# Performance work log

Hardware: AMD Instinct MI355X
Metric: run time of the kernel (lower is better)

The kernel has to match this reference:

```python
import jax, jax.numpy as jnp
import numpy as np

H = 8        # heads
DH = 64      # dim_head
EPS = 1e-5   # LayerNorm eps (torch default)


def setup_inputs() -> dict:
    key = jax.random.key(0)
    k0, k1, k2, k3, k4 = jax.random.split(key, 5)
    b, l, n, dim = 2, 8, 256, 512
    inner = H * DH
    return {
        "xyzs": jax.random.normal(k0, (b, l, n, 3), dtype=jnp.float32),
        "features": jax.random.normal(k1, (b, l, n, dim), dtype=jnp.float32),
        "ln_gamma": jnp.ones((dim,), dtype=jnp.float32),
        "ln_beta": jnp.zeros((dim,), dtype=jnp.float32),
        "w_qkv": jax.random.normal(k2, (dim, 3 * inner), dtype=jnp.float32) * 0.02,
        "w_sp": jax.random.normal(k3, (3, DH), dtype=jnp.float32) * 0.3,
        "w_out": jax.random.normal(k4, (inner, dim), dtype=jnp.float32) * 0.02,
        "b_out": jnp.zeros((dim,), dtype=jnp.float32),
    }


def reference(xyzs, features, ln_gamma, ln_beta, w_qkv, w_sp, w_out, b_out):
    b, l, n, dim = features.shape
    m = l * n
    inner = H * DH
    scale = DH ** (-0.5)

    # LayerNorm over last dim (biased variance, eps=1e-5)
    mu = jnp.mean(features, axis=-1, keepdims=True)
    var = jnp.var(features, axis=-1, keepdims=True)
    normed = (features - mu) * jax.lax.rsqrt(var + EPS) * ln_gamma + ln_beta

    # qkv projection, chunk into q,k,v, reshape 'b l n (h d) -> b h (l n) d'
    qkv = normed.reshape(b, m, dim) @ w_qkv            # [b, m, 3*inner]
    def split_heads(t):
        return t.reshape(b, m, H, DH).transpose(0, 2, 1, 3)  # [b, h, m, d]
    q = split_heads(qkv[..., :inner])
    k = split_heads(qkv[..., inner:2 * inner])
    v = split_heads(qkv[..., 2 * inner:])

    dots = jnp.einsum('bhid,bhjd->bhij', q, k) * scale  # [b, h, m, m]
    attn = jax.nn.softmax(dots, axis=-1)
    v_out = jnp.einsum('bhij,bhjd->bhid', attn, v)      # [b, h, m, d]

    # pairwise coordinate deltas: delta[b,i,j,c] = xyz[b,j,c] - xyz[b,i,c]
    xyz_f = xyzs.reshape(b, m, 3)
    delta = xyz_f[:, None, :, :] - xyz_f[:, :, None, :]  # [b, m, m, 3]
    # attention-weighted aggregation over j (avoids [b,h,m,m,3] intermediate)
    agg = jnp.einsum('bhij,bijc->bhic', attn, delta)     # [b, h, m, 3]
    disp = agg @ w_sp                                    # [b, h, m, DH]

    out = v_out + disp                                   # [b, h, m, DH]
    out = out.transpose(0, 2, 1, 3).reshape(b, m, inner) # 'b h m d -> b m (h d)'
    out = jax.nn.gelu(out @ w_out + b_out, approximate=False)
    return out.reshape(b, l, n, dim) + features
```

## Files before the change

kernel.cpp:

```cpp
#include <hip/hip_runtime.h>
#include <hip/hip_bf16.h>
#include <math.h>

#define BB   2
#define MM   2048
#define DIM  512
#define NH   8
#define DHd  64
#define NQK  1536
#define ROWS 4096
#define NROW 32768

typedef __hip_bfloat16 bf16;
typedef __attribute__((ext_vector_type(8))) short bf16x8;
typedef __attribute__((ext_vector_type(4))) float f32x4;
typedef __attribute__((ext_vector_type(8))) unsigned short us8;

__device__ __forceinline__ unsigned short f2bf_bits(float x) {
    bf16 h = __float2bfloat16(x);
    return *(unsigned short*)&h;
}
__device__ __forceinline__ float bf2f(unsigned short u) {
    unsigned int v = ((unsigned int)u) << 16;
    return __uint_as_float(v);
}

__global__ __launch_bounds__(256) void transpose_bf16_fused(
    const float* __restrict__ wqkv, const float* __restrict__ wout,
    unsigned short* __restrict__ wqkvT, unsigned short* __restrict__ woutT)
{
    __shared__ float st[64][65];
    int by = blockIdx.y;
    const float* in; unsigned short* out; int N, n0;
    if (by < 24) { in = wqkv; out = wqkvT; N = NQK; n0 = by * 64; }
    else         { in = wout; out = woutT; N = DIM; n0 = (by - 24) * 64; }
    int k0 = blockIdx.x * 64;
    int tid = threadIdx.x;
    #pragma unroll
    for (int p = 0; p < 16; p++) {
        int e = tid + p * 256;
        int r = e >> 6, c = e & 63;
        st[r][c] = in[(size_t)(k0 + r) * N + n0 + c];
    }
    __syncthreads();
    #pragma unroll
    for (int p = 0; p < 16; p++) {
        int e = tid + p * 256;
        int nr = e >> 6, kc = e & 63;
        out[(size_t)(n0 + nr) * DIM + k0 + kc] = f2bf_bits(st[kc][nr]);
    }
}

__global__ __launch_bounds__(256) void ln_kernel(
    const float* __restrict__ feat, const float* __restrict__ gamma,
    const float* __restrict__ beta, unsigned short* __restrict__ normed)
{
    int row = blockIdx.x;
    int tid = threadIdx.x;
    const float* fr = feat + (size_t)row * DIM;
    float x0 = fr[tid];
    float x1 = fr[tid + 256];
    float s  = x0 + x1;
    float ss = x0 * x0 + x1 * x1;
    #pragma unroll
    for (int o = 32; o >= 1; o >>= 1) { s += __shfl_down(s, o); ss += __shfl_down(ss, o); }
    __shared__ float ws_[4], wss_[4];
    int wid = tid >> 6, lane = tid & 63;
    if (lane == 0) { ws_[wid] = s; wss_[wid] = ss; }
    __syncthreads();
    if (tid == 0) {
        float a = 0.f, b = 0.f;
        for (int i = 0; i < 4; i++) { a += ws_[i]; b += wss_[i]; }
        ws_[0] = a; wss_[0] = b;
    }
    __syncthreads();
    float mu  = ws_[0] * (1.0f / DIM);
    float var = wss_[0] * (1.0f / DIM) - mu * mu;
    float inv = rsqrtf(var + 1e-5f);
    normed[(size_t)row * DIM + tid]       = f2bf_bits((x0 - mu) * inv * gamma[tid] + beta[tid]);
    normed[(size_t)row * DIM + tid + 256] = f2bf_bits((x1 - mu) * inv * gamma[tid + 256] + beta[tid + 256]);
}

__global__ __launch_bounds__(256) void qkv_gemm(
    const unsigned short* __restrict__ A, const unsigned short* __restrict__ BT,
    unsigned short* __restrict__ qd, unsigned short* __restrict__ kd,
    unsigned short* __restrict__ vd)
{
    __shared__ __align__(16) unsigned short sA[128 * 40];
    __shared__ __align__(16) unsigned short sB[128 * 40];
    int tid = threadIdx.x;
    int r0 = blockIdx.x * 128;
    int n0 = blockIdx.y * 128;
    int chunk = n0 >> 9;
    int cl    = n0 & 511;
    int w = tid >> 6, lane = tid & 63;
    int wm = w >> 1, wn = w & 1;
    int ln15 = lane & 15, quad = lane >> 4;

    int srow = tid >> 1;
    int scol = (tid & 1) * 16;

    f32x4 acc[4][4] = {};

    for (int k0 = 0; k0 < DIM; k0 += 32) {
        __syncthreads();
        *(us8*)&sA[srow * 40 + scol]     = *(const us8*)&A[(size_t)(r0 + srow) * DIM + k0 + scol];
        *(us8*)&sA[srow * 40 + scol + 8] = *(const us8*)&A[(size_t)(r0 + srow) * DIM + k0 + scol + 8];
        *(us8*)&sB[srow * 40 + scol]     = *(const us8*)&BT[(size_t)(n0 + srow) * DIM + k0 + scol];
        *(us8*)&sB[srow * 40 + scol + 8] = *(const us8*)&BT[(size_t)(n0 + srow) * DIM + k0 + scol + 8];
        __syncthreads();
        const unsigned short* fa = (chunk == 2) ? sA : sB;
        const unsigned short* fb = (chunk == 2) ? sB : sA;
        bf16x8 af[4], bf_[4];
        #pragma unroll
        for (int i = 0; i < 4; i++)
            af[i] = *(const bf16x8*)&fa[(wm * 64 + i * 16 + ln15) * 40 + quad * 8];
        #pragma unroll
        for (int j = 0; j < 4; j++)
            bf_[j] = *(const bf16x8*)&fb[(wn * 64 + j * 16 + ln15) * 40 + quad * 8];
        #pragma unroll
        for (int i = 0; i < 4; i++)
            #pragma unroll
            for (int j = 0; j < 4; j++)
                acc[i][j] = __builtin_amdgcn_mfma_f32_16x16x32_bf16(af[i], bf_[j], acc[i][j], 0, 0, 0);
    }

    if (chunk == 2) {
        int rowb = r0 + wm * 64 + quad * 4;
        #pragma unroll
        for (int j = 0; j < 4; j++) {
            int c = cl + wn * 64 + j * 16 + ln15;
            int h = c >> 6, d = c & 63;
            #pragma unroll
            for (int i = 0; i < 4; i++) {
                int gr = rowb + i * 16;
                int bb = gr >> 11, mm = gr & 2047;
                ushort4 pk;
                pk.x = f2bf_bits(acc[i][j][0]);
                pk.y = f2bf_bits(acc[i][j][1]);
                pk.z = f2bf_bits(acc[i][j][2]);
                pk.w = f2bf_bits(acc[i][j][3]);
                *(ushort4*)&vd[((size_t)(bb * NH + h) * DHd + d) * MM + mm] = pk;
            }
        }
    } else {
        unsigned short* dst = (chunk == 0) ? qd : kd;
        float sc = (chunk == 0) ? 0.125f : 1.0f;
        #pragma unroll
        for (int i = 0; i < 4; i++) {
            int within0 = cl + wm * 64 + i * 16 + quad * 4;
            int h = within0 >> 6, d = within0 & 63;
            #pragma unroll
            for (int j = 0; j < 4; j++) {
                int gr = r0 + wn * 64 + j * 16 + ln15;
                int bb = gr >> 11, mm = gr & 2047;
                ushort4 pk;
                pk.x = f2bf_bits(acc[i][j][0] * sc);
                pk.y = f2bf_bits(acc[i][j][1] * sc);
                pk.z = f2bf_bits(acc[i][j][2] * sc);
                pk.w = f2bf_bits(acc[i][j][3] * sc);
                *(ushort4*)&dst[((size_t)(bb * NH + h) * MM + mm) * DHd + d] = pk;
            }
        }
    }
}

__global__ __launch_bounds__(256) void attn_kernel(
    const unsigned short* __restrict__ qg, const unsigned short* __restrict__ kg,
    const unsigned short* __restrict__ vg, const float* __restrict__ xyzs,
    unsigned short* __restrict__ obuf, float* __restrict__ lbuf)
{
    __shared__ __align__(16) unsigned short sQ[64 * 72];
    __shared__ __align__(16) unsigned short sK[64 * 72];
    __shared__ __align__(16) unsigned short sVT[80 * 72];
    __shared__ __align__(16) unsigned short sP[64 * 72];

    int tid = threadIdx.x;
    int bh = blockIdx.y; int bb = bh >> 3;
    int i0 = blockIdx.x * 64;
    int ks = blockIdx.z;
    int w = tid >> 6;
    int lane = tid & 63;
    int ln15 = lane & 15;
    int quad = lane >> 4;

    for (int e = tid; e < 12 * 72; e += 256) sVT[68 * 72 + e] = 0;
    if (tid < 64) sVT[67 * 72 + tid] = 0x3F80;

    {
        const unsigned short* src = qg + ((size_t)bh * MM + i0) * DHd;
        int row = tid >> 2, col = (tid & 3) * 16;
        *(us8*)&sQ[row * 72 + col]     = *(const us8*)&src[(size_t)tid * 16];
        *(us8*)&sQ[row * 72 + col + 8] = *(const us8*)&src[(size_t)tid * 16 + 8];
    }
    asm volatile("s_waitcnt lgkmcnt(0)" ::: "memory");
    bf16x8 aq0 = *(const bf16x8*)&sQ[(w * 16 + ln15) * 72 + quad * 8];
    bf16x8 aq1 = *(const bf16x8*)&sQ[(w * 16 + ln15) * 72 + 32 + quad * 8];

    f32x4 o[5] = {};

    const unsigned short* kbase = kg + (size_t)bh * MM * DHd;
    const unsigned short* vbase = vg + (size_t)bh * DHd * MM;
    int jbeg = ks * (MM / 2), jend = jbeg + (MM / 2);

    int swzr = (ln15 >> 2) << 4;
    int pr0 = (quad * 8) ^ swzr;
    int pr1 = (32 + quad * 8) ^ swzr;
    int pwb = quad << 4;

    for (int jt = jbeg; jt < jend; jt += 64) {
        __syncthreads();
        {
            const unsigned short* src = kbase + (size_t)jt * DHd;
            int row = tid >> 2, col = (tid & 3) * 16;
            *(us8*)&sK[row * 72 + col]     = *(const us8*)&src[(size_t)tid * 16];
            *(us8*)&sK[row * 72 + col + 8] = *(const us8*)&src[(size_t)tid * 16 + 8];
        }
        {
            const unsigned short* src = vbase + jt;
            int d = tid >> 2, koff = (tid & 3) * 16;
            *(us8*)&sVT[d * 72 + koff]     = *(const us8*)&src[(size_t)d * MM + koff];
            *(us8*)&sVT[d * 72 + koff + 8] = *(const us8*)&src[(size_t)d * MM + koff + 8];
        }
        if (tid < 192) {
            int key = tid / 3, c = tid - key * 3;
            float x = xyzs[((size_t)bb * MM + jt) * 3 + tid];
            sVT[(64 + c) * 72 + key] = f2bf_bits(x);
        }
        __syncthreads();

        f32x4 sacc[4];
        #pragma unroll
        for (int t = 0; t < 4; t++) {
            bf16x8 bk0 = *(const bf16x8*)&sK[(t * 16 + ln15) * 72 + quad * 8];
            bf16x8 bk1 = *(const bf16x8*)&sK[(t * 16 + ln15) * 72 + 32 + quad * 8];
            f32x4 z = {};
            z = __builtin_amdgcn_mfma_f32_16x16x32_bf16(aq0, bk0, z, 0, 0, 0);
            z = __builtin_amdgcn_mfma_f32_16x16x32_bf16(aq1, bk1, z, 0, 0, 0);
            sacc[t] = z;
        }

        #pragma unroll
        for (int t = 0; t < 4; t++) {
            int colb = (t * 16) ^ pwb;
            #pragma unroll
            for (int reg = 0; reg < 4; reg++) {
                float pv = __expf(sacc[t][reg]);
                sP[(w * 16 + quad * 4 + reg) * 72 + colb + ln15] = f2bf_bits(pv);
            }
        }
        asm volatile("s_waitcnt lgkmcnt(0)" ::: "memory");
        bf16x8 ap0 = *(const bf16x8*)&sP[(w * 16 + ln15) * 72 + pr0];
        bf16x8 ap1 = *(const bf16x8*)&sP[(w * 16 + ln15) * 72 + pr1];
        #pragma unroll
        for (int t = 0; t < 5; t++) {
            bf16x8 bv0 = *(const bf16x8*)&sVT[(t * 16 + ln15) * 72 + quad * 8];
            bf16x8 bv1 = *(const bf16x8*)&sVT[(t * 16 + ln15) * 72 + 32 + quad * 8];
            o[t] = __builtin_amdgcn_mfma_f32_16x16x32_bf16(ap0, bv0, o[t], 0, 0, 0);
            o[t] = __builtin_amdgcn_mfma_f32_16x16x32_bf16(ap1, bv1, o[t], 0, 0, 0);
        }
    }

    size_t kso = (size_t)ks * NROW;
    #pragma unroll
    for (int reg = 0; reg < 4; reg++) {
        size_t row = (size_t)bh * MM + i0 + w * 16 + quad * 4 + reg;
        unsigned short* orow = obuf + (kso + row) * 72;
        #pragma unroll
        for (int t = 0; t < 4; t++)
            orow[t * 16 + ln15] = f2bf_bits(o[t][reg]);
        if (ln15 < 3)  orow[64 + ln15] = f2bf_bits(o[4][reg]);
        if (ln15 == 3) lbuf[kso + row] = o[4][reg];
    }
}

__global__ __launch_bounds__(256) void merge_kernel(
    const unsigned short* __restrict__ obuf, const float* __restrict__ lbuf,
    const float* __restrict__ xyzs, const float* __restrict__ wsp,
    unsigned short* __restrict__ attn_out)
{
    __shared__ float sW[3][64];
    int tid = threadIdx.x;
    if (tid < 192) sW[tid >> 6][tid & 63] = wsp[tid];
    __syncthreads();
    int r   = blockIdx.x * 64 + (tid >> 2);
    int d0  = (tid & 3) * 16;
    int bh = r >> 11, qrow = r & 2047, bb = bh >> 3, hh = bh & 7;
    const unsigned short* p1 = obuf + (size_t)r * 72;
    const unsigned short* p2 = obuf + ((size_t)NROW + r) * 72;
    float invl = 1.f / (lbuf[r] + lbuf[NROW + r]);
    size_t xb = ((size_t)bb * MM + qrow) * 3;
    float gx = (bf2f(p1[64]) + bf2f(p2[64])) * invl - xyzs[xb + 0];
    float gy = (bf2f(p1[65]) + bf2f(p2[65])) * invl - xyzs[xb + 1];
    float gz = (bf2f(p1[66]) + bf2f(p2[66])) * invl - xyzs[xb + 2];
    us8 a0 = *(const us8*)&p1[d0];
    us8 a1 = *(const us8*)&p1[d0 + 8];
    us8 b0 = *(const us8*)&p2[d0];
    us8 b1 = *(const us8*)&p2[d0 + 8];
    unsigned short outv[16];
    #pragma unroll
    for (int e = 0; e < 8; e++) {
        int d = d0 + e;
        float v = (bf2f(a0[e]) + bf2f(b0[e])) * invl
                + gx * sW[0][d] + gy * sW[1][d] + gz * sW[2][d];
        outv[e] = f2bf_bits(v);
    }
    #pragma unroll
    for (int e = 0; e < 8; e++) {
        int d = d0 + 8 + e;
        float v = (bf2f(a1[e]) + bf2f(b1[e])) * invl
                + gx * sW[0][d] + gy * sW[1][d] + gz * sW[2][d];
        outv[8 + e] = f2bf_bits(v);
    }
    unsigned short* dst = attn_out + ((size_t)bb * MM + qrow) * DIM + hh * DHd + d0;
    *(us8*)dst       = *(us8*)&outv[0];
    *(us8*)(dst + 8) = *(us8*)&outv[8];
}

__global__ __launch_bounds__(256) void out_gemm(
    const unsigned short* __restrict__ A, const unsigned short* __restrict__ BT,
    const float* __restrict__ bias, const float* __restrict__ feat,
    float* __restrict__ out)
{
    __shared__ __align__(16) unsigned short sA[128 * 40];
    __shared__ __align__(16) unsigned short sB[64 * 40];
    int tid = threadIdx.x;
    int r0 = blockIdx.x * 128, n0 = blockIdx.y * 64;
    int w = tid >> 6, lane = tid & 63;
    int ln15 = lane & 15, quad = lane >> 4;

    int srowA = tid >> 1, scolA = (tid & 1) * 16;
    int srowB = tid >> 2, scolB = (tid & 3) * 8;

    f32x4 acc[2][4] = {};

    for (int k0 = 0; k0 < DIM; k0 += 32) {
        __syncthreads();
        *(us8*)&sA[srowA * 40 + scolA]     = *(const us8*)&A[(size_t)(r0 + srowA) * DIM + k0 + scolA];
        *(us8*)&sA[srowA * 40 + scolA + 8] = *(const us8*)&A[(size_t)(r0 + srowA) * DIM + k0 + scolA + 8];
        *(us8*)&sB[srowB * 40 + scolB]     = *(const us8*)&BT[(size_t)(n0 + srowB) * DIM + k0 + scolB];
        __syncthreads();
        bf16x8 af[2], bf_[4];
        #pragma unroll
        for (int i = 0; i < 2; i++)
            af[i] = *(const bf16x8*)&sA[(w * 32 + i * 16 + ln15) * 40 + quad * 8];
        #pragma unroll
        for (int j = 0; j < 4; j++)
            bf_[j] = *(const bf16x8*)&sB[(j * 16 + ln15) * 40 + quad * 8];
        #pragma unroll
        for (int i = 0; i < 2; i++)
            #pragma unroll
            for (int j = 0; j < 4; j++)
                acc[i][j] = __builtin_amdgcn_mfma_f32_16x16x32_bf16(af[i], bf_[j], acc[i][j], 0, 0, 0);
    }

    #pragma unroll
    for (int i = 0; i < 2; i++) {
        #pragma unroll
        for (int reg = 0; reg < 4; reg++) {
            int gr = r0 + w * 32 + i * 16 + quad * 4 + reg;
            #pragma unroll
            for (int j = 0; j < 4; j++) {
                int c = n0 + j * 16 + ln15;
                float x = acc[i][j][reg] + bias[c];
                float g = 0.5f * x * (1.f + erff(x * 0.70710678118f));
                out[(size_t)gr * DIM + c] = g + feat[(size_t)gr * DIM + c];
            }
        }
    }
}

extern "C" void kernel_launch(void* const* d_in, const int* in_sizes, int n_in,
                              void* d_out, int out_size, void* d_ws, size_t ws_size,
                              hipStream_t stream)
{
    const float* xyzs  = (const float*)d_in[0];
    const float* feat  = (const float*)d_in[1];
    const float* gamma = (const float*)d_in[2];
    const float* beta  = (const float*)d_in[3];
    const float* wqkv  = (const float*)d_in[4];
    const float* wsp   = (const float*)d_in[5];
    const float* wout  = (const float*)d_in[6];
    const float* bout  = (const float*)d_in[7];
    float* out = (float*)d_out;

    unsigned short* ws16 = (unsigned short*)d_ws;
    const size_t SEGS = (size_t)ROWS * DIM;
    unsigned short* normed = ws16;
    unsigned short* qb     = ws16 + SEGS;
    unsigned short* kb     = ws16 + 2 * SEGS;
    unsigned short* vb     = ws16 + 3 * SEGS;
    unsigned short* wqkvT  = ws16 + 4 * SEGS;
    unsigned short* woutT  = wqkvT + (size_t)NQK * DIM;
    unsigned short* obuf   = woutT + (size_t)DIM * DIM;
    float*          lbuf   = (float*)(obuf + (size_t)2 * NROW * 72);

    transpose_bf16_fused<<<dim3(8, 32), 256, 0, stream>>>(wqkv, wout, wqkvT, woutT);
    ln_kernel<<<ROWS, 256, 0, stream>>>(feat, gamma, beta, normed);
    qkv_gemm<<<dim3(32, 12), 256, 0, stream>>>(normed, wqkvT, qb, kb, vb);
    attn_kernel<<<dim3(32, 16, 2), 256, 0, stream>>>(qb, kb, vb, xyzs, obuf, lbuf);
    merge_kernel<<<512, 256, 0, stream>>>(obuf, lbuf, xyzs, wsp, normed);
    out_gemm<<<dim3(32, 8), 256, 0, stream>>>(normed, woutT, bout, feat, out);
}
```

Before: 163.9 us.

## Fuse LN with weight transpose, register-prefetch attention tiles, shrink out_gemm tiles

Merges the LayerNorm and weight-transpose kernels into one launch so a kernel boundary disappears. The attention loop now prefetches the next K/V/xyz tile into registers while the current tile is computed, hiding global load latency behind MFMA work. The output GEMM tile drops from 128x64 to 64x64 with a 2x2 warp layout, doubling the block count for better CU occupancy. The cost is more register pressure in attention and less data reuse per block in out_gemm.

```diff
diff --git a/kernel.cpp b/kernel.cpp
--- a/kernel.cpp
+++ b/kernel.cpp
@@ -25,17 +25,45 @@
     return __uint_as_float(v);
 }
 
-__global__ __launch_bounds__(256) void transpose_bf16_fused(
+__global__ __launch_bounds__(256) void pre_kernel(
+    const float* __restrict__ feat, const float* __restrict__ gamma,
+    const float* __restrict__ beta, unsigned short* __restrict__ normed,
     const float* __restrict__ wqkv, const float* __restrict__ wout,
     unsigned short* __restrict__ wqkvT, unsigned short* __restrict__ woutT)
 {
     __shared__ float st[64][65];
-    int by = blockIdx.y;
+    int b = blockIdx.x;
+    int tid = threadIdx.x;
+    if (b < ROWS) {
+        const float* fr = feat + (size_t)b * DIM;
+        float x0 = fr[tid];
+        float x1 = fr[tid + 256];
+        float s  = x0 + x1;
+        float ss = x0 * x0 + x1 * x1;
+        #pragma unroll
+        for (int o = 32; o >= 1; o >>= 1) { s += __shfl_down(s, o); ss += __shfl_down(ss, o); }
+        __shared__ float ws_[4], wss_[4];
+        int wid = tid >> 6, lane = tid & 63;
+        if (lane == 0) { ws_[wid] = s; wss_[wid] = ss; }
+        __syncthreads();
+        if (tid == 0) {
+            float a = 0.f, c = 0.f;
+            for (int i = 0; i < 4; i++) { a += ws_[i]; c += wss_[i]; }
+            ws_[0] = a; wss_[0] = c;
+        }
+        __syncthreads();
+        float mu  = ws_[0] * (1.0f / DIM);
+        float var = wss_[0] * (1.0f / DIM) - mu * mu;
+        float inv = rsqrtf(var + 1e-5f);
+        normed[(size_t)b * DIM + tid]       = f2bf_bits((x0 - mu) * inv * gamma[tid] + beta[tid]);
+        normed[(size_t)b * DIM + tid + 256] = f2bf_bits((x1 - mu) * inv * gamma[tid + 256] + beta[tid + 256]);
+        return;
+    }
+    int idx = b - ROWS;
     const float* in; unsigned short* out; int N, n0;
-    if (by < 24) { in = wqkv; out = wqkvT; N = NQK; n0 = by * 64; }
-    else         { in = wout; out = woutT; N = DIM; n0 = (by - 24) * 64; }
-    int k0 = blockIdx.x * 64;
-    int tid = threadIdx.x;
+    if (idx < 192) { in = wqkv; out = wqkvT; N = NQK; n0 = (idx >> 3) * 64; }
+    else { idx -= 192; in = wout; out = woutT; N = DIM; n0 = (idx >> 3) * 64; }
+    int k0 = (idx & 7) * 64;
     #pragma unroll
     for (int p = 0; p < 16; p++) {
         int e = tid + p * 256;
@@ -49,36 +77,6 @@
         int nr = e >> 6, kc = e & 63;
         out[(size_t)(n0 + nr) * DIM + k0 + kc] = f2bf_bits(st[kc][nr]);
     }
-}
-
-__global__ __launch_bounds__(256) void ln_kernel(
-    const float* __restrict__ feat, const float* __restrict__ gamma,
-    const float* __restrict__ beta, unsigned short* __restrict__ normed)
-{
-    int row = blockIdx.x;
-    int tid = threadIdx.x;
-    const float* fr = feat + (size_t)row * DIM;
-    float x0 = fr[tid];
-    float x1 = fr[tid + 256];
-    float s  = x0 + x1;
-    float ss = x0 * x0 + x1 * x1;
-    #pragma unroll
-    for (int o = 32; o >= 1; o >>= 1) { s += __shfl_down(s, o); ss += __shfl_down(ss, o); }
-    __shared__ float ws_[4], wss_[4];
-    int wid = tid >> 6, lane = tid & 63;
-    if (lane == 0) { ws_[wid] = s; wss_[wid] = ss; }
-    __syncthreads();
-    if (tid == 0) {
-        float a = 0.f, b = 0.f;
-        for (int i = 0; i < 4; i++) { a += ws_[i]; b += wss_[i]; }
-        ws_[0] = a; wss_[0] = b;
-    }
-    __syncthreads();
-    float mu  = ws_[0] * (1.0f / DIM);
-    float var = wss_[0] * (1.0f / DIM) - mu * mu;
-    float inv = rsqrtf(var + 1e-5f);
-    normed[(size_t)row * DIM + tid]       = f2bf_bits((x0 - mu) * inv * gamma[tid] + beta[tid]);
-    normed[(size_t)row * DIM + tid + 256] = f2bf_bits((x1 - mu) * inv * gamma[tid + 256] + beta[tid + 256]);
 }
 
 __global__ __launch_bounds__(256) void qkv_gemm(
@@ -203,31 +201,46 @@
     const unsigned short* vbase = vg + (size_t)bh * DHd * MM;
     int jbeg = ks * (MM / 2), jend = jbeg + (MM / 2);
 
+    int srow = tid >> 2, scol16 = (tid & 3) * 16;
+
+    us8 rk0, rk1, rv0, rv1;
+    float rx = 0.f;
+    {
+        const unsigned short* src = kbase + (size_t)jbeg * DHd;
+        rk0 = *(const us8*)&src[(size_t)tid * 16];
+        rk1 = *(const us8*)&src[(size_t)tid * 16 + 8];
+        const unsigned short* vs = vbase + jbeg;
+        rv0 = *(const us8*)&vs[(size_t)srow * MM + scol16];
+        rv1 = *(const us8*)&vs[(size_t)srow * MM + scol16 + 8];
+        if (tid < 192) rx = xyzs[((size_t)bb * MM + jbeg) * 3 + tid];
+    }
+
+    int pwb = quad << 4;
     int swzr = (ln15 >> 2) << 4;
     int pr0 = (quad * 8) ^ swzr;
     int pr1 = (32 + quad * 8) ^ swzr;
-    int pwb = quad << 4;
 
     for (int jt = jbeg; jt < jend; jt += 64) {
         __syncthreads();
-        {
-            const unsigned short* src = kbase + (size_t)jt * DHd;
-            int row = tid >> 2, col = (tid & 3) * 16;
-            *(us8*)&sK[row * 72 + col]     = *(const us8*)&src[(size_t)tid * 16];
-            *(us8*)&sK[row * 72 + col + 8] = *(const us8*)&src[(size_t)tid * 16 + 8];
-        }
-        {
-            const unsigned short* src = vbase + jt;
-            int d = tid >> 2, koff = (tid & 3) * 16;
-            *(us8*)&sVT[d * 72 + koff]     = *(const us8*)&src[(size_t)d * MM + koff];
-            *(us8*)&sVT[d * 72 + koff + 8] = *(const us8*)&src[(size_t)d * MM + koff + 8];
-        }
+        *(us8*)&sK[srow * 72 + scol16]      = rk0;
+        *(us8*)&sK[srow * 72 + scol16 + 8]  = rk1;
+        *(us8*)&sVT[srow * 72 + scol16]     = rv0;
+        *(us8*)&sVT[srow * 72 + scol16 + 8] = rv1;
         if (tid < 192) {
             int key = tid / 3, c = tid - key * 3;
-            float x = xyzs[((size_t)bb * MM + jt) * 3 + tid];
-            sVT[(64 + c) * 72 + key] = f2bf_bits(x);
-        }
-        __syncthreads();
+            sVT[(64 + c) * 72 + key] = f2bf_bits(rx);
+        }
+        __syncthreads();
+        int jn = jt + 64;
+        if (jn < jend) {
+            const unsigned short* src = kbase + (size_t)jn * DHd;
+            rk0 = *(const us8*)&src[(size_t)tid * 16];
+            rk1 = *(const us8*)&src[(size_t)tid * 16 + 8];
+            const unsigned short* vs = vbase + jn;
+            rv0 = *(const us8*)&vs[(size_t)srow * MM + scol16];
+            rv1 = *(const us8*)&vs[(size_t)srow * MM + scol16 + 8];
+            if (tid < 192) rx = xyzs[((size_t)bb * MM + jn) * 3 + tid];
+        }
 
         f32x4 sacc[4];
         #pragma unroll
@@ -322,35 +335,34 @@
     const float* __restrict__ bias, const float* __restrict__ feat,
     float* __restrict__ out)
 {
-    __shared__ __align__(16) unsigned short sA[128 * 40];
+    __shared__ __align__(16) unsigned short sA[64 * 40];
     __shared__ __align__(16) unsigned short sB[64 * 40];
     int tid = threadIdx.x;
-    int r0 = blockIdx.x * 128, n0 = blockIdx.y * 64;
+    int r0 = blockIdx.x * 64, n0 = blockIdx.y * 64;
     int w = tid >> 6, lane = tid & 63;
+    int wm = w >> 1, wn = w & 1;
     int ln15 = lane & 15, quad = lane >> 4;
 
-    int srowA = tid >> 1, scolA = (tid & 1) * 16;
-    int srowB = tid >> 2, scolB = (tid & 3) * 8;
-
-    f32x4 acc[2][4] = {};
+    int srow = tid >> 2, scol = (tid & 3) * 8;
+
+    f32x4 acc[2][2] = {};
 
     for (int k0 = 0; k0 < DIM; k0 += 32) {
         __syncthreads();
-        *(us8*)&sA[srowA * 40 + scolA]     = *(const us8*)&A[(size_t)(r0 + srowA) * DIM + k0 + scolA];
-        *(us8*)&sA[srowA * 40 + scolA + 8] = *(const us8*)&A[(size_t)(r0 + srowA) * DIM + k0 + scolA + 8];
-        *(us8*)&sB[srowB * 40 + scolB]     = *(const us8*)&BT[(size_t)(n0 + srowB) * DIM + k0 + scolB];
-        __syncthreads();
-        bf16x8 af[2], bf_[4];
+        *(us8*)&sA[srow * 40 + scol] = *(const us8*)&A[(size_t)(r0 + srow) * DIM + k0 + scol];
+        *(us8*)&sB[srow * 40 + scol] = *(const us8*)&BT[(size_t)(n0 + srow) * DIM + k0 + scol];
+        __syncthreads();
+        bf16x8 af[2], bf_[2];
         #pragma unroll
         for (int i = 0; i < 2; i++)
-            af[i] = *(const bf16x8*)&sA[(w * 32 + i * 16 + ln15) * 40 + quad * 8];
-        #pragma unroll
-        for (int j = 0; j < 4; j++)
-            bf_[j] = *(const bf16x8*)&sB[(j * 16 + ln15) * 40 + quad * 8];
+            af[i] = *(const bf16x8*)&sA[(wm * 32 + i * 16 + ln15) * 40 + quad * 8];
+        #pragma unroll
+        for (int j = 0; j < 2; j++)
+            bf_[j] = *(const bf16x8*)&sB[(wn * 32 + j * 16 + ln15) * 40 + quad * 8];
         #pragma unroll
         for (int i = 0; i < 2; i++)
             #pragma unroll
-            for (int j = 0; j < 4; j++)
+            for (int j = 0; j < 2; j++)
                 acc[i][j] = __builtin_amdgcn_mfma_f32_16x16x32_bf16(af[i], bf_[j], acc[i][j], 0, 0, 0);
     }
 
@@ -358,10 +370,10 @@
     for (int i = 0; i < 2; i++) {
         #pragma unroll
         for (int reg = 0; reg < 4; reg++) {
-            int gr = r0 + w * 32 + i * 16 + quad * 4 + reg;
-            #pragma unroll
-            for (int j = 0; j < 4; j++) {
-                int c = n0 + j * 16 + ln15;
+            int gr = r0 + wm * 32 + i * 16 + quad * 4 + reg;
+            #pragma unroll
+            for (int j = 0; j < 2; j++) {
+                int c = n0 + wn * 32 + j * 16 + ln15;
                 float x = acc[i][j][reg] + bias[c];
                 float g = 0.5f * x * (1.f + erff(x * 0.70710678118f));
                 out[(size_t)gr * DIM + c] = g + feat[(size_t)gr * DIM + c];
@@ -395,10 +407,10 @@
     unsigned short* obuf   = woutT + (size_t)DIM * DIM;
     float*          lbuf   = (float*)(obuf + (size_t)2 * NROW * 72);
 
-    transpose_bf16_fused<<<dim3(8, 32), 256, 0, stream>>>(wqkv, wout, wqkvT, woutT);
-    ln_kernel<<<ROWS, 256, 0, stream>>>(feat, gamma, beta, normed);
+    pre_kernel<<<ROWS + 256, 256, 0, stream>>>(feat, gamma, beta, normed,
+                                               wqkv, wout, wqkvT, woutT);
     qkv_gemm<<<dim3(32, 12), 256, 0, stream>>>(normed, wqkvT, qb, kb, vb);
     attn_kernel<<<dim3(32, 16, 2), 256, 0, stream>>>(qb, kb, vb, xyzs, obuf, lbuf);
     merge_kernel<<<512, 256, 0, stream>>>(obuf, lbuf, xyzs, wsp, normed);
-    out_gemm<<<dim3(32, 8), 256, 0, stream>>>(normed, woutT, bout, feat, out);
-}
+    out_gemm<<<dim3(64, 8), 256, 0, stream>>>(normed, woutT, bout, feat, out);
+}
```

Result: faster. 154.5 us (-5.7%).
